# Kernel optimization log

Measured on AMD Instinct MI355X. Metric: run time of the kernel, lower is better.

The kernel has to match this reference:

```python
import jax, jax.numpy as jnp
import numpy as np

N_NODES = 50000
N_EDGES = 800000
F_DIM = 128   # float_feat_dim
H_DIM = 64    # hidden_dim
NEG_SLOPE = 0.2


def setup_inputs() -> dict:
    key = jax.random.key(0)
    ks = jax.random.split(key, 12)
    in_dim = F_DIM + 1
    sc_in = 1.0 / np.sqrt(in_dim)
    sc_h = 1.0 / np.sqrt(H_DIM)
    return {
        "x_float": jax.random.normal(ks[0], (N_NODES, F_DIM), dtype=jnp.float32),
        "x_binary": jax.random.uniform(ks[1], (N_NODES,), dtype=jnp.float32),
        "edge_index": jax.random.randint(ks[2], (2, N_EDGES), 0, N_NODES, dtype=jnp.int64),
        "Wl": jax.random.normal(ks[3], (H_DIM, in_dim), dtype=jnp.float32) * sc_in,
        "bl": jnp.zeros((H_DIM,), dtype=jnp.float32),
        "Wr": jax.random.normal(ks[4], (H_DIM, in_dim), dtype=jnp.float32) * sc_in,
        "br": jnp.zeros((H_DIM,), dtype=jnp.float32),
        "att": jax.random.normal(ks[5], (H_DIM,), dtype=jnp.float32) * sc_h,
        "gat_bias": jnp.zeros((H_DIM,), dtype=jnp.float32),
        "Wo": jax.random.normal(ks[6], (F_DIM, H_DIM), dtype=jnp.float32) * sc_h,
        "bo": jnp.zeros((F_DIM,), dtype=jnp.float32),
        "dispersion": jnp.zeros((F_DIM,), dtype=jnp.float32),
    }


def reference(x_float, x_binary, edge_index, Wl, bl, Wr, br, att, gat_bias, Wo, bo, dispersion):
    N = x_float.shape[0]
    # concat float feats with binary feature -> [N, F+1]
    x = jnp.concatenate([x_float, x_binary[:, None]], axis=1)
    # add self loops (PyG GATv2Conv default)
    loops = jnp.arange(N, dtype=edge_index.dtype)
    src = jnp.concatenate([edge_index[0], loops])  # [E+N]
    dst = jnp.concatenate([edge_index[1], loops])
    # separate source/target linear projections (share_weights=False)
    xl = x @ Wl.T + bl  # [N, H]
    xr = x @ Wr.T + br  # [N, H]
    # per-edge GATv2 attention score: a^T LeakyReLU(x_l[j] + x_r[i])
    m = xl[src] + xr[dst]                      # [E+N, H]
    m = jnp.where(m > 0, m, NEG_SLOPE * m)
    e = m @ att                                # [E+N]
    # segment softmax over destination neighborhoods
    emax = jax.ops.segment_max(e, dst, num_segments=N)  # self loops => every seg nonempty
    ex = jnp.exp(e - emax[dst])
    denom = jax.ops.segment_sum(ex, dst, num_segments=N)
    alpha = ex / denom[dst]                    # [E+N]
    # weighted scatter-aggregate of source projections
    out = jax.ops.segment_sum(alpha[:, None] * xl[src], dst, num_segments=N) + gat_bias
    h = jax.nn.elu(out)                        # [N, H]
    logits = h @ Wo.T + bo                     # [N, F]
    return logits, jax.nn.softplus(dispersion)
```

## Files before the change

### kernel.cpp

```cpp
#include <hip/hip_runtime.h>
#include <hip/hip_bf16.h>
#include <math.h>

#define N_NODES 50000
#define N_EDGES 800000
#define F_DIM 128
#define H_DIM 64
#define IN_DIM 129
#define ETOT (N_EDGES + N_NODES)
#define PROJ_BLKS ((N_NODES + 31) / 32)
#define OUT_BLKS  ((N_NODES + 31) / 32)
#define NB 196
#define CAP 6144
#define EPB 3125

typedef __hip_bfloat16 bf16;
typedef __attribute__((ext_vector_type(8))) short bf16x8;
typedef __attribute__((ext_vector_type(4))) float f32x4;

static __device__ __forceinline__ float bs2f(short s) {
    union { float f; unsigned u; } c; c.u = ((unsigned)(unsigned short)s) << 16; return c.f;
}
static __device__ __forceinline__ short f2bs(float f) {
    union { bf16 b; short s; } u; u.b = __float2bfloat16(f); return u.s;
}

__global__ __launch_bounds__(256) void prep_kernel(
    const float* __restrict__ Wl, const float* __restrict__ Wr,
    const float* __restrict__ Wo,
    bf16* __restrict__ whi, bf16* __restrict__ wlo,
    bf16* __restrict__ wohi, bf16* __restrict__ wolo,
    int* __restrict__ gcur)
{
    int b = blockIdx.x, t = threadIdx.x;
    if (b < 8) {
        int s = b * 256 + t;
        int fid = s >> 6, l = s & 63;
        int wave = fid >> 3, nt = (fid >> 2) & 1, ks = fid & 3;
        int ch = wave * 32 + nt * 16 + (l & 15);
        int kb = ks * 32 + (l >> 4) * 8;
        const float* wrow = (ch < 64) ? Wl + (size_t)ch * IN_DIM
                                      : Wr + (size_t)(ch - 64) * IN_DIM;
        #pragma unroll
        for (int j = 0; j < 8; ++j) {
            float v = wrow[kb + j];
            short hs = f2bs(v);
            short ls = f2bs(v - bs2f(hs));
            ((short*)whi)[(size_t)s * 8 + j] = hs;
            ((short*)wlo)[(size_t)s * 8 + j] = ls;
        }
    } else if (b < 12) {
        int s = (b - 8) * 256 + t;
        int fid = s >> 6, l = s & 63;
        int wave = fid >> 2, nt = (fid >> 1) & 1, ks = fid & 1;
        int ch = wave * 32 + nt * 16 + (l & 15);
        int kb = ks * 32 + (l >> 4) * 8;
        const float* wrow = Wo + (size_t)ch * H_DIM;
        #pragma unroll
        for (int j = 0; j < 8; ++j) {
            float v = wrow[kb + j];
            short hs = f2bs(v);
            short ls = f2bs(v - bs2f(hs));
            ((short*)wohi)[(size_t)s * 8 + j] = hs;
            ((short*)wolo)[(size_t)s * 8 + j] = ls;
        }
    } else {
        if (t < NB) gcur[t] = 0;
    }
}

__global__ __launch_bounds__(1024) void bucket_kernel(
    const int* __restrict__ esrc, const int* __restrict__ edst,
    int* __restrict__ gcur, unsigned* __restrict__ bstore)
{
    __shared__ unsigned ent[EPB];
    __shared__ int hist[NB], lbase[NB], c2[NB];
    int t = threadIdx.x;
    if (t < NB) hist[t] = 0;
    __syncthreads();

    int e0 = blockIdx.x * EPB;
    for (int k = t; k < EPB; k += 1024) {
        int dst = edst[e0 + k];
        unsigned en = ((unsigned)dst << 16) | (unsigned)esrc[e0 + k];
        ent[k] = en;
        atomicAdd(&hist[dst >> 8], 1);
    }
    __syncthreads();

    if (t < NB) {
        int hh = hist[t];
        lbase[t] = hh ? atomicAdd(&gcur[t], hh) : 0;
        c2[t] = 0;
    }
    __syncthreads();

    for (int k = t; k < EPB; k += 1024) {
        unsigned en = ent[k];
        int j = en >> 24;
        int r = atomicAdd(&c2[j], 1);
        bstore[(size_t)j * CAP + lbase[j] + r] = en;
    }
}

__global__ __launch_bounds__(256) void csr_kernel(
    const int* __restrict__ gcur, const unsigned* __restrict__ bstore,
    int* __restrict__ offs, int* __restrict__ csr_src)
{
    __shared__ unsigned ent[CAP];
    __shared__ int sh[256], h256[256], start[256], c2[256];
    __shared__ int bb_s, C_s;
    int j = blockIdx.x, t = threadIdx.x;

    int val = 0;
    if (t < NB) val = gcur[t] + ((t < NB - 1) ? 256 : (N_NODES - (NB - 1) * 256));
    sh[t] = val;
    __syncthreads();
    #pragma unroll
    for (int d = 1; d < 256; d <<= 1) {
        int x = (t >= d) ? sh[t - d] : 0;
        __syncthreads();
        sh[t] += x;
        __syncthreads();
    }
    if (t == j) bb_s = sh[t] - val;
    if (t == 0) C_s = gcur[j];
    h256[t] = 0;
    __syncthreads();
    int bb = bb_s, C = C_s;

    for (int k = t; k < C; k += 256) {
        unsigned en = bstore[(size_t)j * CAP + k];
        ent[k] = en;
        atomicAdd(&h256[(en >> 16) & 255], 1);
    }
    __syncthreads();

    int node = j * 256 + t;
    int w = h256[t] + ((node < N_NODES) ? 1 : 0);
    sh[t] = w;
    __syncthreads();
    #pragma unroll
    for (int d = 1; d < 256; d <<= 1) {
        int x = (t >= d) ? sh[t - d] : 0;
        __syncthreads();
        sh[t] += x;
        __syncthreads();
    }
    int st = bb + sh[t] - w;
    start[t] = st;
    c2[t] = 0;
    if (node < N_NODES) {
        offs[node] = st;
        csr_src[st] = node;
    }
    if (j == NB - 1 && t == 0) offs[N_NODES] = ETOT;
    __syncthreads();

    for (int k = t; k < C; k += 256) {
        unsigned en = ent[k];
        int bin = (en >> 16) & 255;
        int r = atomicAdd(&c2[bin], 1);
        csr_src[start[bin] + 1 + r] = (int)(en & 0xffffu);
    }
}

__global__ __launch_bounds__(256) void proj_mfma(
    const float* __restrict__ xf, const float* __restrict__ xb,
    const float* __restrict__ Wl, const float* __restrict__ bl,
    const float* __restrict__ Wr, const float* __restrict__ br,
    const bf16* __restrict__ whi, const bf16* __restrict__ wlo,
    bf16* __restrict__ xl, bf16* __restrict__ xr)
{
    __shared__ short lds[32 * 128];

    int wave = threadIdx.x >> 6;
    int lane = threadIdx.x & 63;
    int n = lane & 15, q = lane >> 4;
    int node0 = blockIdx.x * 32;

    bf16x8 bhi[2][4], blo_[2][4];
    float biasv[2], w128[2];
    #pragma unroll
    for (int nt = 0; nt < 2; ++nt) {
        int ch = wave * 32 + nt * 16 + n;
        #pragma unroll
        for (int ks = 0; ks < 4; ++ks) {
            int fid = wave * 8 + nt * 4 + ks;
            bhi[nt][ks]  = *(const bf16x8*)(whi + ((size_t)fid * 64 + lane) * 8);
            blo_[nt][ks] = *(const bf16x8*)(wlo + ((size_t)fid * 64 + lane) * 8);
        }
        biasv[nt] = (ch < 64) ? bl[ch] : br[ch - 64];
        w128[nt]  = (ch < 64) ? Wl[(size_t)ch * IN_DIM + 128]
                              : Wr[(size_t)(ch - 64) * IN_DIM + 128];
    }

    #pragma unroll
    for (int mt = 0; mt < 2; ++mt) {
        int nb = node0 + mt * 16;
        if (nb < N_NODES) {
            const float* xrow = xf + (size_t)(nb + n) * F_DIM;
            bf16x8 a[4];
            #pragma unroll
            for (int ks = 0; ks < 4; ++ks) {
                float4 u = *(const float4*)(xrow + ks * 32 + q * 8);
                float4 v = *(const float4*)(xrow + ks * 32 + q * 8 + 4);
                bf16x8 tt;
                tt[0] = f2bs(u.x); tt[1] = f2bs(u.y); tt[2] = f2bs(u.z); tt[3] = f2bs(u.w);
                tt[4] = f2bs(v.x); tt[5] = f2bs(v.y); tt[6] = f2bs(v.z); tt[7] = f2bs(v.w);
                a[ks] = tt;
            }
            f32x4 acc[2] = {{0.f,0.f,0.f,0.f},{0.f,0.f,0.f,0.f}};
            #pragma unroll
            for (int ks = 0; ks < 4; ++ks) {
                #pragma unroll
                for (int nt = 0; nt < 2; ++nt) {
                    acc[nt] = __builtin_amdgcn_mfma_f32_16x16x32_bf16(a[ks], bhi[nt][ks],  acc[nt], 0, 0, 0);
                    acc[nt] = __builtin_amdgcn_mfma_f32_16x16x32_bf16(a[ks], blo_[nt][ks], acc[nt], 0, 0, 0);
                }
            }
            float4 xbv = *(const float4*)(xb + nb + q * 4);
            float xbr[4] = {xbv.x, xbv.y, xbv.z, xbv.w};
            #pragma unroll
            for (int nt = 0; nt < 2; ++nt) {
                int ch = wave * 32 + nt * 16 + n;
                int blk = ch >> 3, pos = ch & 7;
                #pragma unroll
                for (int r = 0; r < 4; ++r) {
                    int nodeL = mt * 16 + q * 4 + r;
                    float val = acc[nt][r] + xbr[r] * w128[nt] + biasv[nt];
                    lds[nodeL * 128 + ((blk ^ (nodeL & 7)) << 3) + pos] = f2bs(val);
                }
            }
        }
    }
    __syncthreads();

    int nl = threadIdx.x >> 3, bk = threadIdx.x & 7;
    int node = node0 + nl;
    if (node < N_NODES) {
        bf16x8 v0 = *(const bf16x8*)(lds + nl * 128 + ((bk ^ (nl & 7)) << 3));
        *(bf16x8*)(xl + (size_t)node * H_DIM + bk * 8) = v0;
        bf16x8 v1 = *(const bf16x8*)(lds + nl * 128 + (((8 + bk) ^ (nl & 7)) << 3));
        *(bf16x8*)(xr + (size_t)node * H_DIM + bk * 8) = v1;
    }
}

__global__ __launch_bounds__(256) void agg_fused(
    const int* __restrict__ csr_src, const int* __restrict__ offs,
    const bf16* __restrict__ xl, const bf16* __restrict__ xr,
    const float* __restrict__ att, const float* __restrict__ gb,
    bf16* __restrict__ h)
{
    int wid  = (blockIdx.x * 256 + threadIdx.x) >> 6;
    int lane = threadIdx.x & 63;
    if (wid >= N_NODES) return;
    int g  = lane >> 3;
    int c8 = lane & 7;

    float attv[8], xrv[8];
    {
        bf16x8 xrow = *(const bf16x8*)(xr + (size_t)wid * H_DIM + c8 * 8);
        float4 a0 = *(const float4*)(att + c8 * 8);
        float4 a1 = *(const float4*)(att + c8 * 8 + 4);
        attv[0] = a0.x; attv[1] = a0.y; attv[2] = a0.z; attv[3] = a0.w;
        attv[4] = a1.x; attv[5] = a1.y; attv[6] = a1.z; attv[7] = a1.w;
        #pragma unroll
        for (int j = 0; j < 8; ++j) xrv[j] = bs2f(xrow[j]);
    }

    int beg = offs[wid];
    int end = offs[wid + 1];
    int last = end - 1;
    float den = 0.f;
    float acc[8] = {0.f, 0.f, 0.f, 0.f, 0.f, 0.f, 0.f, 0.f};

    int i0 = beg + g;        i0 = (i0 < end) ? i0 : last;
    int i1 = beg + 8 + g;    i1 = (i1 < end) ? i1 : last;
    int i2 = beg + 16 + g;   i2 = (i2 < end) ? i2 : last;
    int srcC = csr_src[i2];
    bf16x8 xa = *(const bf16x8*)(xl + (size_t)csr_src[i0] * H_DIM + c8 * 8);
    bf16x8 xb = *(const bf16x8*)(xl + (size_t)csr_src[i1] * H_DIM + c8 * 8);

    for (int base = beg; base < end; base += 8) {
        int i3 = base + 24 + g;  i3 = (i3 < end) ? i3 : last;
        int srcD = csr_src[i3];
        bf16x8 xc = *(const bf16x8*)(xl + (size_t)srcC * H_DIM + c8 * 8);

        bool valid = (base + g) < end;
        float xv[8], p = 0.f;
        #pragma unroll
        for (int j = 0; j < 8; ++j) {
            xv[j] = bs2f(xa[j]);
            float m = xv[j] + xrv[j];
            m = (m > 0.f) ? m : 0.2f * m;
            p += m * attv[j];
        }
        p += __shfl_xor(p, 1);
        p += __shfl_xor(p, 2);
        p += __shfl_xor(p, 4);
        float ex = valid ? __expf(p) : 0.f;
        den += ex;
        #pragma unroll
        for (int j = 0; j < 8; ++j) acc[j] += ex * xv[j];

        xa = xb;
        xb = xc;
        srcC = srcD;
    }

    #pragma unroll
    for (int j = 0; j < 8; ++j) {
        acc[j] += __shfl_xor(acc[j], 8);
        acc[j] += __shfl_xor(acc[j], 16);
        acc[j] += __shfl_xor(acc[j], 32);
    }
    den += __shfl_xor(den, 8);
    den += __shfl_xor(den, 16);
    den += __shfl_xor(den, 32);

    if (g == 0) {
        float inv = 1.0f / den;
        float4 g0 = *(const float4*)(gb + c8 * 8);
        float4 g1 = *(const float4*)(gb + c8 * 8 + 4);
        float gbv[8] = {g0.x, g0.y, g0.z, g0.w, g1.x, g1.y, g1.z, g1.w};
        bf16x8 ov;
        #pragma unroll
        for (int j = 0; j < 8; ++j) {
            float v = acc[j] * inv + gbv[j];
            v = (v > 0.f) ? v : expm1f(v);
            ov[j] = f2bs(v);
        }
        *(bf16x8*)(h + (size_t)wid * H_DIM + c8 * 8) = ov;
    }
}

__global__ __launch_bounds__(256) void out_mfma(
    const bf16* __restrict__ h,
    const bf16* __restrict__ wohi, const bf16* __restrict__ wolo,
    const float* __restrict__ bo, const float* __restrict__ disp,
    float* __restrict__ out)
{
    if (blockIdx.x == 0 && threadIdx.x < F_DIM) {
        float d = disp[threadIdx.x];
        out[(size_t)N_NODES * F_DIM + threadIdx.x] = (d > 20.f) ? d : log1pf(__expf(d));
    }

    __shared__ float ldso[32 * 132];

    int wave = threadIdx.x >> 6;
    int lane = threadIdx.x & 63;
    int n = lane & 15, q = lane >> 4;
    int node0 = blockIdx.x * 32;

    bf16x8 bhi[2][2], blo_[2][2];
    float bov[2];
    #pragma unroll
    for (int nt = 0; nt < 2; ++nt) {
        int ch = wave * 32 + nt * 16 + n;
        #pragma unroll
        for (int ks = 0; ks < 2; ++ks) {
            int fid = wave * 4 + nt * 2 + ks;
            bhi[nt][ks]  = *(const bf16x8*)(wohi + ((size_t)fid * 64 + lane) * 8);
            blo_[nt][ks] = *(const bf16x8*)(wolo + ((size_t)fid * 64 + lane) * 8);
        }
        bov[nt] = bo[ch];
    }

    #pragma unroll
    for (int mt = 0; mt < 2; ++mt) {
        int nb = node0 + mt * 16;
        if (nb < N_NODES) {
            const bf16* hrow = h + (size_t)(nb + n) * H_DIM;
            bf16x8 a[2];
            #pragma unroll
            for (int ks = 0; ks < 2; ++ks)
                a[ks] = *(const bf16x8*)(hrow + ks * 32 + q * 8);
            f32x4 acc[2] = {{0.f,0.f,0.f,0.f},{0.f,0.f,0.f,0.f}};
            #pragma unroll
            for (int ks = 0; ks < 2; ++ks) {
                #pragma unroll
                for (int nt = 0; nt < 2; ++nt) {
                    acc[nt] = __builtin_amdgcn_mfma_f32_16x16x32_bf16(a[ks], bhi[nt][ks],  acc[nt], 0, 0, 0);
                    acc[nt] = __builtin_amdgcn_mfma_f32_16x16x32_bf16(a[ks], blo_[nt][ks], acc[nt], 0, 0, 0);
                }
            }
            #pragma unroll
            for (int nt = 0; nt < 2; ++nt) {
                int ch = wave * 32 + nt * 16 + n;
                #pragma unroll
                for (int r = 0; r < 4; ++r) {
                    int nodeL = mt * 16 + q * 4 + r;
                    ldso[nodeL * 132 + ch] = acc[nt][r] + bov[nt];
                }
            }
        }
    }
    __syncthreads();

    int nl = threadIdx.x >> 3, c = threadIdx.x & 7;
    int node = node0 + nl;
    if (node < N_NODES) {
        const float* srcp = ldso + nl * 132 + c * 16;
        float* dstp = out + (size_t)node * F_DIM + c * 16;
        #pragma unroll
        for (int i = 0; i < 4; ++i)
            *(float4*)(dstp + i * 4) = *(const float4*)(srcp + i * 4);
    }
}

extern "C" void kernel_launch(void* const* d_in, const int* in_sizes, int n_in,
                              void* d_out, int out_size, void* d_ws, size_t ws_size,
                              hipStream_t stream)
{
    const float* xf  = (const float*)d_in[0];
    const float* xb  = (const float*)d_in[1];
    const int*   ei  = (const int*)d_in[2];
    const float* Wl  = (const float*)d_in[3];
    const float* bl  = (const float*)d_in[4];
    const float* Wr  = (const float*)d_in[5];
    const float* br  = (const float*)d_in[6];
    const float* att = (const float*)d_in[7];
    const float* gb  = (const float*)d_in[8];
    const float* Wo  = (const float*)d_in[9];
    const float* bo  = (const float*)d_in[10];
    const float* dp  = (const float*)d_in[11];
    float* out = (float*)d_out;
    const int* esrc = ei;
    const int* edst = ei + N_EDGES;

    char* ws = (char*)d_ws;
    const size_t SZB = (size_t)N_NODES * H_DIM * sizeof(bf16);
    bf16*  xl      = (bf16*)(ws);
    bf16*  xr      = (bf16*)(ws + SZB);
    bf16*  h       = (bf16*)(ws + 2 * SZB);
    unsigned* bstore = (unsigned*)h;
    int*   csr_src = (int*)(ws + 3 * SZB);
    int*   offs    = (int*)(ws + 3 * SZB + (size_t)ETOT * 4);
    int*   gcur    = offs + (N_NODES + 4);
    bf16*  whi     = (bf16*)(gcur + NB + 12);
    bf16*  wlo     = whi + 16384;
    bf16*  wohi    = wlo + 16384;
    bf16*  wolo    = wohi + 8192;

    prep_kernel<<<13, 256, 0, stream>>>(Wl, Wr, Wo, whi, wlo, wohi, wolo, gcur);

    bucket_kernel<<<256, 1024, 0, stream>>>(esrc, edst, gcur, bstore);

    csr_kernel<<<NB, 256, 0, stream>>>(gcur, bstore, offs, csr_src);

    proj_mfma<<<PROJ_BLKS, 256, 0, stream>>>(xf, xb, Wl, bl, Wr, br,
                                             whi, wlo, xl, xr);

    agg_fused<<<(N_NODES * 64) / 256, 256, 0, stream>>>(csr_src, offs,
                                                        xl, xr, att, gb, h);

    out_mfma<<<OUT_BLKS, 256, 0, stream>>>(h, wohi, wolo, bo, dp, out);
}
```

Measured before the change: 190.8 us.

## Merge edge bucketing into projection kernel and widen CSR blocks

Combines the edge bucketing pass and the node projection MFMA kernel into one launch: extra blocks past the projection range do the bucket histogram and scatter on smaller edge chunks of 256 threads. This lets the two independent stages run concurrently and removes a launch boundary. The CSR build kernel now uses 512 threads so the bucket load and scatter loops use more threads, while the scans still use 256. Each bucketing block now issues more global atomics per edge, and smaller chunks mean more contention on gcur.

```diff
diff --git a/kernel.cpp b/kernel.cpp
--- a/kernel.cpp
+++ b/kernel.cpp
@@ -12,7 +12,8 @@
 #define OUT_BLKS  ((N_NODES + 31) / 32)
 #define NB 196
 #define CAP 6144
-#define EPB 3125
+#define EPB2 782
+#define BKT_BLKS 1024
 
 typedef __hip_bfloat16 bf16;
 typedef __attribute__((ext_vector_type(8))) short bf16x8;
@@ -69,110 +70,52 @@
     }
 }
 
-__global__ __launch_bounds__(1024) void bucket_kernel(
-    const int* __restrict__ esrc, const int* __restrict__ edst,
-    int* __restrict__ gcur, unsigned* __restrict__ bstore)
-{
-    __shared__ unsigned ent[EPB];
-    __shared__ int hist[NB], lbase[NB], c2[NB];
-    int t = threadIdx.x;
-    if (t < NB) hist[t] = 0;
-    __syncthreads();
-
-    int e0 = blockIdx.x * EPB;
-    for (int k = t; k < EPB; k += 1024) {
-        int dst = edst[e0 + k];
-        unsigned en = ((unsigned)dst << 16) | (unsigned)esrc[e0 + k];
-        ent[k] = en;
-        atomicAdd(&hist[dst >> 8], 1);
-    }
-    __syncthreads();
-
-    if (t < NB) {
-        int hh = hist[t];
-        lbase[t] = hh ? atomicAdd(&gcur[t], hh) : 0;
-        c2[t] = 0;
-    }
-    __syncthreads();
-
-    for (int k = t; k < EPB; k += 1024) {
-        unsigned en = ent[k];
-        int j = en >> 24;
-        int r = atomicAdd(&c2[j], 1);
-        bstore[(size_t)j * CAP + lbase[j] + r] = en;
-    }
-}
-
-__global__ __launch_bounds__(256) void csr_kernel(
-    const int* __restrict__ gcur, const unsigned* __restrict__ bstore,
-    int* __restrict__ offs, int* __restrict__ csr_src)
-{
-    __shared__ unsigned ent[CAP];
-    __shared__ int sh[256], h256[256], start[256], c2[256];
-    __shared__ int bb_s, C_s;
-    int j = blockIdx.x, t = threadIdx.x;
-
-    int val = 0;
-    if (t < NB) val = gcur[t] + ((t < NB - 1) ? 256 : (N_NODES - (NB - 1) * 256));
-    sh[t] = val;
-    __syncthreads();
-    #pragma unroll
-    for (int d = 1; d < 256; d <<= 1) {
-        int x = (t >= d) ? sh[t - d] : 0;
-        __syncthreads();
-        sh[t] += x;
-        __syncthreads();
-    }
-    if (t == j) bb_s = sh[t] - val;
-    if (t == 0) C_s = gcur[j];
-    h256[t] = 0;
-    __syncthreads();
-    int bb = bb_s, C = C_s;
-
-    for (int k = t; k < C; k += 256) {
-        unsigned en = bstore[(size_t)j * CAP + k];
-        ent[k] = en;
-        atomicAdd(&h256[(en >> 16) & 255], 1);
-    }
-    __syncthreads();
-
-    int node = j * 256 + t;
-    int w = h256[t] + ((node < N_NODES) ? 1 : 0);
-    sh[t] = w;
-    __syncthreads();
-    #pragma unroll
-    for (int d = 1; d < 256; d <<= 1) {
-        int x = (t >= d) ? sh[t - d] : 0;
-        __syncthreads();
-        sh[t] += x;
-        __syncthreads();
-    }
-    int st = bb + sh[t] - w;
-    start[t] = st;
-    c2[t] = 0;
-    if (node < N_NODES) {
-        offs[node] = st;
-        csr_src[st] = node;
-    }
-    if (j == NB - 1 && t == 0) offs[N_NODES] = ETOT;
-    __syncthreads();
-
-    for (int k = t; k < C; k += 256) {
-        unsigned en = ent[k];
-        int bin = (en >> 16) & 255;
-        int r = atomicAdd(&c2[bin], 1);
-        csr_src[start[bin] + 1 + r] = (int)(en & 0xffffu);
-    }
-}
-
-__global__ __launch_bounds__(256) void proj_mfma(
+__global__ __launch_bounds__(256) void h1_kernel(
     const float* __restrict__ xf, const float* __restrict__ xb,
     const float* __restrict__ Wl, const float* __restrict__ bl,
     const float* __restrict__ Wr, const float* __restrict__ br,
     const bf16* __restrict__ whi, const bf16* __restrict__ wlo,
-    bf16* __restrict__ xl, bf16* __restrict__ xr)
-{
-    __shared__ short lds[32 * 128];
+    const int* __restrict__ esrc, const int* __restrict__ edst,
+    bf16* __restrict__ xl, bf16* __restrict__ xr,
+    int* __restrict__ gcur, unsigned* __restrict__ bstore)
+{
+    __shared__ int smem[2048];
+
+    if (blockIdx.x >= PROJ_BLKS) {
+        unsigned* ent = (unsigned*)smem;
+        int* hist  = smem + 782;
+        int* lbase = smem + 978;
+        int* c2    = smem + 1174;
+        int t = threadIdx.x;
+        if (t < NB) hist[t] = 0;
+        __syncthreads();
+
+        int e0 = (blockIdx.x - PROJ_BLKS) * EPB2;
+        int cnt = N_EDGES - e0; if (cnt > EPB2) cnt = EPB2;
+        for (int k = t; k < cnt; k += 256) {
+            int dst = edst[e0 + k];
+            ent[k] = ((unsigned)dst << 16) | (unsigned)esrc[e0 + k];
+            atomicAdd(&hist[dst >> 8], 1);
+        }
+        __syncthreads();
+
+        if (t < NB) {
+            int hh = hist[t];
+            lbase[t] = hh ? atomicAdd(&gcur[t], hh) : 0;
+            c2[t] = 0;
+        }
+        __syncthreads();
+
+        for (int k = t; k < cnt; k += 256) {
+            unsigned en = ent[k];
+            int j = en >> 24;
+            int r = atomicAdd(&c2[j], 1);
+            bstore[(size_t)j * CAP + lbase[j] + r] = en;
+        }
+        return;
+    }
+
+    short* lds = (short*)smem;
 
     int wave = threadIdx.x >> 6;
     int lane = threadIdx.x & 63;
@@ -243,6 +186,73 @@
         *(bf16x8*)(xl + (size_t)node * H_DIM + bk * 8) = v0;
         bf16x8 v1 = *(const bf16x8*)(lds + nl * 128 + (((8 + bk) ^ (nl & 7)) << 3));
         *(bf16x8*)(xr + (size_t)node * H_DIM + bk * 8) = v1;
+    }
+}
+
+__global__ __launch_bounds__(512) void csr_kernel(
+    const int* __restrict__ gcur, const unsigned* __restrict__ bstore,
+    int* __restrict__ offs, int* __restrict__ csr_src)
+{
+    __shared__ unsigned ent[CAP];
+    __shared__ int sh[256], h256[256], start[256], c2[256];
+    __shared__ int bb_s, C_s;
+    int j = blockIdx.x, t = threadIdx.x;
+
+    int val = 0;
+    if (t < NB) val = gcur[t] + ((t < NB - 1) ? 256 : (N_NODES - (NB - 1) * 256));
+    if (t < 256) sh[t] = val;
+    __syncthreads();
+    #pragma unroll
+    for (int d = 1; d < 256; d <<= 1) {
+        int x = (t >= d && t < 256) ? sh[t - d] : 0;
+        __syncthreads();
+        if (t < 256) sh[t] += x;
+        __syncthreads();
+    }
+    if (t == j) bb_s = sh[t] - val;
+    if (t == 0) C_s = gcur[j];
+    if (t < 256) h256[t] = 0;
+    __syncthreads();
+    int bb = bb_s, C = C_s;
+
+    for (int k = t; k < C; k += 512) {
+        unsigned en = bstore[(size_t)j * CAP + k];
+        ent[k] = en;
+        atomicAdd(&h256[(en >> 16) & 255], 1);
+    }
+    __syncthreads();
+
+    int w = 0;
+    if (t < 256) {
+        w = h256[t] + ((j * 256 + t < N_NODES) ? 1 : 0);
+        sh[t] = w;
+    }
+    __syncthreads();
+    #pragma unroll
+    for (int d = 1; d < 256; d <<= 1) {
+        int x = (t >= d && t < 256) ? sh[t - d] : 0;
+        __syncthreads();
+        if (t < 256) sh[t] += x;
+        __syncthreads();
+    }
+    if (t < 256) {
+        int st = bb + sh[t] - w;
+        start[t] = st;
+        c2[t] = 0;
+        int node = j * 256 + t;
+        if (node < N_NODES) {
+            offs[node] = st;
+            csr_src[st] = node;
+        }
+    }
+    if (j == NB - 1 && t == 0) offs[N_NODES] = ETOT;
+    __syncthreads();
+
+    for (int k = t; k < C; k += 512) {
+        unsigned en = ent[k];
+        int bin = (en >> 16) & 255;
+        int r = atomicAdd(&c2[bin], 1);
+        csr_src[start[bin] + 1 + r] = (int)(en & 0xffffu);
     }
 }
 
@@ -445,12 +455,10 @@
 
     prep_kernel<<<13, 256, 0, stream>>>(Wl, Wr, Wo, whi, wlo, wohi, wolo, gcur);
 
-    bucket_kernel<<<256, 1024, 0, stream>>>(esrc, edst, gcur, bstore);
-
-    csr_kernel<<<NB, 256, 0, stream>>>(gcur, bstore, offs, csr_src);
-
-    proj_mfma<<<PROJ_BLKS, 256, 0, stream>>>(xf, xb, Wl, bl, Wr, br,
-                                             whi, wlo, xl, xr);
+    h1_kernel<<<PROJ_BLKS + BKT_BLKS, 256, 0, stream>>>(
+        xf, xb, Wl, bl, Wr, br, whi, wlo, esrc, edst, xl, xr, gcur, bstore);
+
+    csr_kernel<<<NB, 512, 0, stream>>>(gcur, bstore, offs, csr_src);
 
     agg_fused<<<(N_NODES * 64) / 256, 256, 0, stream>>>(csr_src, offs,
                                                         xl, xr, att, gb, h);
```

Result: slower. 198.0 us (+3.8%).
